# Performance work log

Hardware: AMD Instinct MI355X
Metric: run time of the kernel (lower is better)

## Reference

```python
import jax, jax.numpy as jnp
import numpy as np

B, S, H = 1, 2048, 1024
NH, NKV, HD = 16, 4, 64
E, F, TOPK = 8, 2048, 2
EPS = 1e-6
ALPHA = 1.702
LIMIT = 7.0


def setup_inputs() -> dict:
    key = jax.random.key(0)
    ks = jax.random.split(key, 16)
    sc = 0.02
    inv_freq = 1.0 / (10000.0 ** (jnp.arange(0, HD, 2, dtype=jnp.float32) / HD))  # [HD/2]
    pos = jnp.arange(S, dtype=jnp.float32)[:, None] * inv_freq[None, :]  # [S, HD/2]
    causal = jnp.tril(jnp.ones((S, S), dtype=bool))
    mask = jnp.where(causal, 0.0, -1e9).astype(jnp.float32)[None, None]  # [1,1,S,S]
    return {
        "hidden_states": jax.random.normal(ks[0], (B, S, H), jnp.float32),
        "sins": jnp.sin(pos),
        "coss": jnp.cos(pos),
        "mask": mask,
        "ln1_w": jnp.ones((H,), jnp.float32),
        "ln2_w": jnp.ones((H,), jnp.float32),
        "wq": jax.random.normal(ks[1], (H, NH * HD), jnp.float32) * sc,
        "wk": jax.random.normal(ks[2], (H, NKV * HD), jnp.float32) * sc,
        "wv": jax.random.normal(ks[3], (H, NKV * HD), jnp.float32) * sc,
        "wo": jax.random.normal(ks[4], (NH * HD, H), jnp.float32) * sc,
        "w_router": jax.random.normal(ks[5], (H, E), jnp.float32) * sc,
        "b_router": jnp.zeros((E,), jnp.float32),
        "gate_up_proj": jax.random.normal(ks[6], (E, H, 2 * F), jnp.float32) * sc,
        "gate_up_bias": jnp.zeros((E, 2 * F), jnp.float32),
        "down_proj": jax.random.normal(ks[7], (E, F, H), jnp.float32) * sc,
        "down_bias": jnp.zeros((E, H), jnp.float32),
    }


def _rmsnorm(x, w):
    x = x.astype(jnp.float32)
    var = jnp.mean(x * x, axis=-1, keepdims=True)
    return x * jax.lax.rsqrt(var + EPS) * w


def _rope(x, sins, coss):
    # x: [B, S, nH, HD]; sins/coss: [S, HD/2]
    d = x.shape[-1] // 2
    xr, xi = x[..., :d], x[..., d:]
    s = sins[None, : x.shape[1], None, :]
    c = coss[None, : x.shape[1], None, :]
    return jnp.concatenate([xr * c - xi * s, xr * s + xi * c], axis=-1)


def reference(hidden_states, sins, coss, mask, ln1_w, ln2_w, wq, wk, wv, wo,
              w_router, b_router, gate_up_proj, gate_up_bias, down_proj, down_bias):
    # ---- attention block ----
    residual = hidden_states
    x = _rmsnorm(hidden_states, ln1_w)
    q = (x @ wq).reshape(B, S, NH, HD)
    k = (x @ wk).reshape(B, S, NKV, HD)
    v = (x @ wv).reshape(B, S, NKV, HD)
    q = _rope(q, sins, coss)
    k = _rope(k, sins, coss)
    groups = NH // NKV
    k = jnp.repeat(k, groups, axis=2)  # [B,S,NH,HD]
    v = jnp.repeat(v, groups, axis=2)
    scale = 1.0 / jnp.sqrt(jnp.float32(HD))
    scores = jnp.einsum("bqhd,bkhd->bhqk", q, k) * scale + mask
    probs = jax.nn.softmax(scores, axis=-1)
    attn = jnp.einsum("bhqk,bkhd->bqhd", probs, v).reshape(B, S, NH * HD)
    hidden = residual + attn @ wo

    # ---- MoE block ----
    residual = hidden
    x = _rmsnorm(hidden, ln2_w)
    flat = x.reshape(-1, H)  # [N, H], N = B*S
    logits = flat @ w_router + b_router  # [N, E]
    top_val, top_idx = jax.lax.top_k(logits, TOPK)
    top_val = jax.nn.softmax(top_val, axis=-1)
    scores_r = jnp.zeros_like(logits)
    token_idx = jnp.arange(B * S)[:, None]
    scores_r = scores_r.at[token_idx, top_idx].set(top_val)  # [N, E]

    # dense all-expert FFN (faithful to original)
    gate_up = jnp.einsum("nh,ehd->end", flat, gate_up_proj) + gate_up_bias[:, None, :]
    gate = jnp.minimum(gate_up[..., ::2], LIMIT)
    up = jnp.clip(gate_up[..., 1::2], -LIMIT, LIMIT)
    glu = gate * jax.nn.sigmoid(gate * ALPHA)
    gated = (up + 1.0) * glu  # [E, N, F]
    next_states = jnp.einsum("end,edh->enh", gated, down_proj) + down_bias[:, None, :]
    weights = scores_r.T  # [E, N]
    moe_out = jnp.sum(next_states * weights[..., None], axis=0).reshape(B, S, H)

    return residual + moe_out
```

## Files before the change

kernel.cpp:

```cpp
#include <hip/hip_runtime.h>
#include <hip/hip_bf16.h>
#include <math.h>

#define SS 2048
#define HH 1024
#define NHEADS 16
#define NKVH 4
#define HDIM 64
#define NEXP 8
#define FDIM 2048

static constexpr float EPSV   = 1e-6f;
static constexpr float ALPHAV = 1.702f;
static constexpr float LIMITV = 7.0f;

typedef __attribute__((ext_vector_type(8))) short bf16x8;
typedef __attribute__((ext_vector_type(4))) float f32x4;

__device__ __forceinline__ float wave_reduce_sum(float v) {
#pragma unroll
  for (int off = 32; off; off >>= 1) v += __shfl_xor(v, off);
  return v;
}

__device__ __forceinline__ unsigned short bf16_bits(float x) {
  __hip_bfloat16 h = __float2bfloat16(x);
  return *reinterpret_cast<unsigned short*>(&h);
}

__device__ __forceinline__ float bf16u_to_f(unsigned short u) {
  union { unsigned int i; float f; } c;
  c.i = ((unsigned int)u) << 16;
  return c.f;
}

__device__ __forceinline__ void gload_lds16(const __hip_bfloat16* g, __hip_bfloat16* s) {
  __builtin_amdgcn_global_load_lds(
      (const __attribute__((address_space(1))) void*)g,
      (__attribute__((address_space(3))) void*)s, 16, 0, 0);
}

__global__ void rmsnorm_kernel(const float* __restrict__ x,
                               const float* __restrict__ w,
                               float* __restrict__ o32,
                               __hip_bfloat16* __restrict__ o16) {
  int row = blockIdx.x;
  int t = threadIdx.x;
  const float4 v = ((const float4*)(x + (size_t)row * HH))[t];
  float ss = v.x * v.x + v.y * v.y + v.z * v.z + v.w * v.w;
  ss = wave_reduce_sum(ss);
  __shared__ float parts[4];
  if ((t & 63) == 0) parts[t >> 6] = ss;
  __syncthreads();
  float tot = parts[0] + parts[1] + parts[2] + parts[3];
  float r = rsqrtf(tot * (1.0f / HH) + EPSV);
  const float4 ww = ((const float4*)w)[t];
  float4 out;
  out.x = v.x * r * ww.x;
  out.y = v.y * r * ww.y;
  out.z = v.z * r * ww.z;
  out.w = v.w * r * ww.w;
  if (o32) ((float4*)(o32 + (size_t)row * HH))[t] = out;
  __hip_bfloat16* d = o16 + (size_t)row * HH + t * 4;
  d[0] = __float2bfloat16(out.x);
  d[1] = __float2bfloat16(out.y);
  d[2] = __float2bfloat16(out.z);
  d[3] = __float2bfloat16(out.w);
}

__device__ __forceinline__ void tcast_body(
    const float* __restrict__ ip, __hip_bfloat16* __restrict__ op,
    int R, int C, int bx, int by, int tid) {
  __shared__ float tile[64][65];
  int c0 = bx * 64, r0 = by * 64;
  int tx = tid & 15, ty = tid >> 4;
#pragma unroll
  for (int j = 0; j < 4; ++j) {
    int row = ty + j * 16;
    float4 v = *(const float4*)(ip + (size_t)(r0 + row) * C + c0 + tx * 4);
    tile[row][tx * 4 + 0] = v.x;
    tile[row][tx * 4 + 1] = v.y;
    tile[row][tx * 4 + 2] = v.z;
    tile[row][tx * 4 + 3] = v.w;
  }
  __syncthreads();
#pragma unroll
  for (int j = 0; j < 4; ++j) {
    int crow = ty + j * 16;
    ushort4 o;
    o.x = bf16_bits(tile[tx * 4 + 0][crow]);
    o.y = bf16_bits(tile[tx * 4 + 1][crow]);
    o.z = bf16_bits(tile[tx * 4 + 2][crow]);
    o.w = bf16_bits(tile[tx * 4 + 3][crow]);
    *(ushort4*)(op + (size_t)(c0 + crow) * R + r0 + tx * 4) = o;
  }
}

__global__ __launch_bounds__(256) void tcast_kernel(
    const float* __restrict__ in, __hip_bfloat16* __restrict__ out,
    int R, int C, size_t inBatch, size_t outBatch) {
  tcast_body(in + blockIdx.z * inBatch, out + blockIdx.z * outBatch,
             R, C, blockIdx.x, blockIdx.y, threadIdx.x);
}

__global__ __launch_bounds__(256) void tcast4_kernel(
    const float* __restrict__ wq, const float* __restrict__ wk,
    const float* __restrict__ wv, const float* __restrict__ wo,
    __hip_bfloat16* __restrict__ qkvT, __hip_bfloat16* __restrict__ woT) {
  int z = blockIdx.z;
  const float* in;
  __hip_bfloat16* out;
  int C;
  if (z == 0)      { in = wq; out = qkvT;                C = 1024; }
  else if (z == 1) { in = wk; out = qkvT + 1024 * 1024;  C = 256; }
  else if (z == 2) { in = wv; out = qkvT + 1280 * 1024;  C = 256; }
  else             { in = wo; out = woT;                 C = 1024; }
  if (blockIdx.x * 64 >= C) return;
  tcast_body(in, out, 1024, C, blockIdx.x, blockIdx.y, threadIdx.x);
}

template <int MODE>
__global__ __launch_bounds__(256, 4) void mfma_gemm(
    const __hip_bfloat16* __restrict__ A,
    const __hip_bfloat16* __restrict__ Bt,
    float* __restrict__ Cf, __hip_bfloat16* __restrict__ Cb,
    const float* __restrict__ addend, const float* __restrict__ bias,
    const int* __restrict__ counts, const int* __restrict__ offsets,
    const int* __restrict__ tos, int M0, int N, int K) {
  int e = blockIdx.z;
  int M = M0, off = 0;
  if (MODE >= 2) { M = counts[e]; off = offsets[e]; }
  int row0 = blockIdx.y * 128;
  if (row0 >= M) return;
  int n0 = blockIdx.x * 128;
  const __hip_bfloat16* Bte = Bt + (size_t)e * ((size_t)N * K);
  __shared__ __align__(16) __hip_bfloat16 sA0[128 * 32];
  __shared__ __align__(16) __hip_bfloat16 sA1[128 * 32];
  __shared__ __align__(16) __hip_bfloat16 sB0[128 * 32];
  __shared__ __align__(16) __hip_bfloat16 sB1[128 * 32];
  int t = threadIdx.x;
  int lane = t & 63;
  int wm = t >> 7, wn = (t >> 6) & 1;
  f32x4 acc[4][4] = {};

  int arow[2];
#pragma unroll
  for (int i = 0; i < 2; ++i) {
    int rg = row0 + i * 64 + (t >> 2);
    int ar;
    if (MODE == 2)      ar = (rg < M) ? tos[off + rg] : tos[off];
    else if (MODE == 3) ar = off + ((rg < M) ? rg : 0);
    else                ar = rg;
    arow[i] = ar;
  }
  int brow0 = n0 + (t >> 2);
  int kc = (t & 3) * 8;

  for (int k0 = 0; k0 < K; k0 += 64) {
#pragma unroll
    for (int i = 0; i < 2; ++i) {
      int r = i * 64 + (t >> 2);
      const __hip_bfloat16* ap = A + (size_t)arow[i] * K + k0 + kc;
      const __hip_bfloat16* bp = Bte + (size_t)(brow0 + i * 64) * K + k0 + kc;
      gload_lds16(ap, sA0 + r * 32 + kc);
      gload_lds16(ap + 32, sA1 + r * 32 + kc);
      gload_lds16(bp, sB0 + r * 32 + kc);
      gload_lds16(bp + 32, sB1 + r * 32 + kc);
    }
    __syncthreads();
#pragma unroll
    for (int half = 0; half < 2; ++half) {
      const __hip_bfloat16* sa = half ? sA1 : sA0;
      const __hip_bfloat16* sb = half ? sB1 : sB0;
      bf16x8 af[4], bfr[4];
#pragma unroll
      for (int mi = 0; mi < 4; ++mi)
        af[mi] = *(const bf16x8*)(sa + (wm * 64 + mi * 16 + (lane & 15)) * 32 + (lane >> 4) * 8);
#pragma unroll
      for (int ni = 0; ni < 4; ++ni)
        bfr[ni] = *(const bf16x8*)(sb + (wn * 64 + ni * 16 + (lane & 15)) * 32 + (lane >> 4) * 8);
#pragma unroll
      for (int mi = 0; mi < 4; ++mi)
#pragma unroll
        for (int ni = 0; ni < 4; ++ni)
          acc[mi][ni] = __builtin_amdgcn_mfma_f32_16x16x32_bf16(af[mi], bfr[ni], acc[mi][ni], 0, 0, 0);
    }
    __syncthreads();
  }

#pragma unroll
  for (int mi = 0; mi < 4; ++mi) {
#pragma unroll
    for (int ni = 0; ni < 4; ++ni) {
      int col = n0 + wn * 64 + ni * 16 + (lane & 15);
#pragma unroll
      for (int j = 0; j < 4; ++j) {
        float v = acc[mi][ni][j];
        int rg = row0 + wm * 64 + mi * 16 + (lane >> 4) * 4 + j;
        if (MODE == 0) {
          Cf[(size_t)rg * N + col] = v;
        } else if (MODE == 1) {
          Cf[(size_t)rg * N + col] = v + addend[(size_t)rg * N + col];
        } else if (MODE == 2) {
          float other = __shfl_xor(v, 1);
          if (!(lane & 1) && rg < M) {
            float gate = fminf(v + bias[(size_t)e * N + col], LIMITV);
            float up = fminf(fmaxf(other + bias[(size_t)e * N + col + 1], -LIMITV), LIMITV);
            float glu = gate / (1.f + __expf(-gate * ALPHAV));
            Cb[(size_t)(off + rg) * (N / 2) + (col >> 1)] = __float2bfloat16((up + 1.f) * glu);
          }
        } else {
          if (rg < M)
            Cf[(size_t)(off + rg) * N + col] = v + bias[(size_t)e * N + col];
        }
      }
    }
  }
}

__global__ __launch_bounds__(512) void rope_cast_kernel(
    const float* __restrict__ qkv, const float* __restrict__ sins,
    const float* __restrict__ coss,
    __hip_bfloat16* __restrict__ qhi, __hip_bfloat16* __restrict__ qlo,
    __hip_bfloat16* __restrict__ khi, __hip_bfloat16* __restrict__ klo) {
  int s = blockIdx.x, t = threadIdx.x;
  const float* rowp = qkv + (size_t)s * 1536;
  int hh = t >> 5, j = t & 31;
  float c = coss[s * 32 + j], sn = sins[s * 32 + j];
  {
    float xr = rowp[hh * 64 + j], xi = rowp[hh * 64 + 32 + j];
    float y0 = xr * c - xi * sn;
    float y1 = xr * sn + xi * c;
    size_t i0 = (size_t)s * 1024 + hh * 64 + j;
    __hip_bfloat16 h0 = __float2bfloat16(y0);
    __hip_bfloat16 h1 = __float2bfloat16(y1);
    qhi[i0] = h0;      qlo[i0] = __float2bfloat16(y0 - __bfloat162float(h0));
    qhi[i0 + 32] = h1; qlo[i0 + 32] = __float2bfloat16(y1 - __bfloat162float(h1));
  }
  if (t < 128) {
    int kh = t >> 5;
    float xr = rowp[1024 + kh * 64 + j], xi = rowp[1024 + kh * 64 + 32 + j];
    float y0 = xr * c - xi * sn;
    float y1 = xr * sn + xi * c;
    size_t i0 = (size_t)kh * 131072 + s * 64 + j;
    __hip_bfloat16 h0 = __float2bfloat16(y0);
    __hip_bfloat16 h1 = __float2bfloat16(y1);
    khi[i0] = h0;      klo[i0] = __float2bfloat16(y0 - __bfloat162float(h0));
    khi[i0 + 32] = h1; klo[i0 + 32] = __float2bfloat16(y1 - __bfloat162float(h1));
  }
}

__global__ void vtrans_kernel(const float* __restrict__ qkv,
                              __hip_bfloat16* __restrict__ vT,
                              int* __restrict__ counts) {
  if (blockIdx.x == 0 && blockIdx.y == 0 && blockIdx.z == 0 && threadIdx.x < 8)
    counts[threadIdx.x] = 0;
  __shared__ float tile[32][33];
  int kh = blockIdx.z;
  int d0 = blockIdx.x * 32;
  int s0 = blockIdx.y * 32;
  int tx = threadIdx.x & 31, ty = threadIdx.x >> 5;
#pragma unroll
  for (int j = 0; j < 4; ++j)
    tile[ty * 4 + j][tx] =
        qkv[(size_t)(s0 + ty * 4 + j) * 1536 + 1280 + kh * 64 + d0 + tx];
  __syncthreads();
#pragma unroll
  for (int j = 0; j < 4; ++j)
    vT[(size_t)kh * 131072 + (size_t)(d0 + ty * 4 + j) * 2048 + s0 + tx] =
        __float2bfloat16(tile[tx][ty * 4 + j]);
}

__device__ __forceinline__ void swsm(
    f32x4* sacc, float (*p)[4], int kv0, bool last, int qr, int g,
    float& m, float& l, float* af4, f32x4* acc_o) {
  float smax = -1e30f;
#pragma unroll
  for (int n = 0; n < 4; ++n)
#pragma unroll
    for (int j = 0; j < 4; ++j) {
      float s = sacc[n][j] * 0.125f;
      if (last && (kv0 + n * 16 + g * 4 + j) > qr) s = -1e30f;
      p[n][j] = s;
      smax = fmaxf(smax, s);
    }
  smax = fmaxf(smax, __shfl_xor(smax, 16));
  smax = fmaxf(smax, __shfl_xor(smax, 32));
  float mnew = fmaxf(m, smax);
  float a = __expf(m - mnew);
  float rs = 0.f;
#pragma unroll
  for (int n = 0; n < 4; ++n)
#pragma unroll
    for (int j = 0; j < 4; ++j) {
      float e2 = __expf(p[n][j] - mnew);
      p[n][j] = e2;
      rs += e2;
    }
  rs += __shfl_xor(rs, 16);
  rs += __shfl_xor(rs, 32);
  l = l * a + rs;
  m = mnew;
#pragma unroll
  for (int j = 0; j < 4; ++j) af4[j] = __shfl(a, g * 4 + j);
#pragma unroll
  for (int n2 = 0; n2 < 4; ++n2)
#pragma unroll
    for (int j = 0; j < 4; ++j) acc_o[n2][j] *= af4[j];
}

__device__ __forceinline__ void build_pfrag(
    float (*p)[4], int s2, int H0, int H1, int nsel, bf16x8& Ah, bf16x8& Al) {
  unsigned int pkh[2][2], pkl[2][2];
#pragma unroll
  for (int nn = 0; nn < 2; ++nn) {
#pragma unroll
    for (int d = 0; d < 2; ++d) {
      float p0 = p[2 * s2 + nn][2 * d], p1 = p[2 * s2 + nn][2 * d + 1];
      unsigned short h0 = bf16_bits(p0), h1 = bf16_bits(p1);
      pkh[nn][d] = (unsigned int)h0 | ((unsigned int)h1 << 16);
      float l0 = p0 - bf16u_to_f(h0), l1 = p1 - bf16u_to_f(h1);
      pkl[nn][d] = (unsigned int)bf16_bits(l0) | ((unsigned int)bf16_bits(l1) << 16);
    }
  }
  union { unsigned int u[4]; bf16x8 v; } AhU, AlU;
#pragma unroll
  for (int d = 0; d < 2; ++d) {
    unsigned int x0 = (unsigned int)__shfl((int)pkh[0][d], H0);
    unsigned int x1 = (unsigned int)__shfl((int)pkh[1][d], H0);
    AhU.u[d] = nsel ? x1 : x0;
    unsigned int y0 = (unsigned int)__shfl((int)pkh[0][d], H1);
    unsigned int y1 = (unsigned int)__shfl((int)pkh[1][d], H1);
    AhU.u[2 + d] = nsel ? y1 : y0;
    unsigned int z0 = (unsigned int)__shfl((int)pkl[0][d], H0);
    unsigned int z1 = (unsigned int)__shfl((int)pkl[1][d], H0);
    AlU.u[d] = nsel ? z1 : z0;
    unsigned int w0 = (unsigned int)__shfl((int)pkl[0][d], H1);
    unsigned int w1 = (unsigned int)__shfl((int)pkl[1][d], H1);
    AlU.u[2 + d] = nsel ? w1 : w0;
  }
  Ah = AhU.v;
  Al = AlU.v;
}

__global__ __launch_bounds__(128) void mfma_attn(
    const __hip_bfloat16* __restrict__ qhi, const __hip_bfloat16* __restrict__ qlo,
    const __hip_bfloat16* __restrict__ khi, const __hip_bfloat16* __restrict__ klo,
    const __hip_bfloat16* __restrict__ vT,
    float* __restrict__ pacc,
    float* __restrict__ pm,
    float* __restrict__ pl) {
  int hp = blockIdx.y;
  int h0 = 2 * hp, h1 = 2 * hp + 1, kh = hp >> 1;
  int ck = blockIdx.z;
  int wq = threadIdx.x >> 6;
  int qb = 2 * blockIdx.x + wq;
  if (16 * ck > qb) return;
  int lane = threadIdx.x & 63;
  int g = lane >> 4, q = lane & 15;
  int qrow0 = qb * 16;
  const int koff = g * 8;

  bf16x8 bqhA[2], bqlA[2], bqhB[2], bqlB[2];
  {
    size_t qoA = (size_t)(qrow0 + q) * 1024 + h0 * 64;
    bqhA[0] = *(const bf16x8*)(qhi + qoA + koff);
    bqhA[1] = *(const bf16x8*)(qhi + qoA + 32 + koff);
    bqlA[0] = *(const bf16x8*)(qlo + qoA + koff);
    bqlA[1] = *(const bf16x8*)(qlo + qoA + 32 + koff);
    size_t qoB = qoA + 64;
    bqhB[0] = *(const bf16x8*)(qhi + qoB + koff);
    bqhB[1] = *(const bf16x8*)(qhi + qoB + 32 + koff);
    bqlB[0] = *(const bf16x8*)(qlo + qoB + koff);
    bqlB[1] = *(const bf16x8*)(qlo + qoB + 32 + koff);
  }
  f32x4 accA[4] = {}, accB[4] = {};
  float mA = -1e30f, lA = 0.f, mB = -1e30f, lB = 0.f;
  const size_t kbase = (size_t)kh * (SS * 64) + (size_t)q * 64 + koff;
  const __hip_bfloat16* khp = khi + kbase;
  const __hip_bfloat16* klp = klo + kbase;
  const __hip_bfloat16* vfp =
      vT + (size_t)kh * (64 * SS) + (size_t)q * SS + koff;

  int ntiles = qb / 4 + 1;
  int lastT = ntiles - 1;
  int t0 = 4 * ck;
  int t1 = 4 * ck + 4; if (t1 > ntiles) t1 = ntiles;

  const int H0s = ((2 * g) & 3) * 16 + q;
  const int H1s = ((2 * g + 1) & 3) * 16 + q;
  const int nsel = (g >> 1) & 1;
  int qr = qrow0 + q;

  for (int tile = t0; tile < t1; ++tile) {
    int kv0 = tile * 64;
    bool last = (tile == lastT);

    bf16x8 kfh[4][2], kfl[4][2];
#pragma unroll
    for (int n = 0; n < 4; ++n)
#pragma unroll
      for (int step = 0; step < 2; ++step) {
        size_t ko = (size_t)(kv0 + n * 16) * 64 + step * 32;
        kfh[n][step] = *(const bf16x8*)(khp + ko);
        kfl[n][step] = *(const bf16x8*)(klp + ko);
      }

    f32x4 sA[4] = {}, sB[4] = {};
    __builtin_amdgcn_s_setprio(1);
#pragma unroll
    for (int n = 0; n < 4; ++n) {
#pragma unroll
      for (int step = 0; step < 2; ++step) {
        sA[n] = __builtin_amdgcn_mfma_f32_16x16x32_bf16(kfh[n][step], bqhA[step], sA[n], 0, 0, 0);
        sB[n] = __builtin_amdgcn_mfma_f32_16x16x32_bf16(kfh[n][step], bqhB[step], sB[n], 0, 0, 0);
        sA[n] = __builtin_amdgcn_mfma_f32_16x16x32_bf16(kfl[n][step], bqhA[step], sA[n], 0, 0, 0);
        sB[n] = __builtin_amdgcn_mfma_f32_16x16x32_bf16(kfl[n][step], bqhB[step], sB[n], 0, 0, 0);
        sA[n] = __builtin_amdgcn_mfma_f32_16x16x32_bf16(kfh[n][step], bqlA[step], sA[n], 0, 0, 0);
        sB[n] = __builtin_amdgcn_mfma_f32_16x16x32_bf16(kfh[n][step], bqlB[step], sB[n], 0, 0, 0);
      }
    }
    __builtin_amdgcn_s_setprio(0);

    bf16x8 vf[4][2];
#pragma unroll
    for (int s2 = 0; s2 < 2; ++s2)
#pragma unroll
      for (int n2 = 0; n2 < 4; ++n2)
        vf[n2][s2] = *(const bf16x8*)(vfp + (size_t)(n2 * 16) * SS + kv0 + s2 * 32);

    float pA[4][4], pB[4][4];
    float af4[4];
    swsm(sA, pA, kv0, last, qr, g, mA, lA, af4, accA);
    swsm(sB, pB, kv0, last, qr, g, mB, lB, af4, accB);

#pragma unroll
    for (int s2 = 0; s2 < 2; ++s2) {
      bf16x8 AhA, AlA, AhB, AlB;
      build_pfrag(pA, s2, H0s, H1s, nsel, AhA, AlA);
      build_pfrag(pB, s2, H0s, H1s, nsel, AhB, AlB);
      __builtin_amdgcn_s_setprio(1);
#pragma unroll
      for (int n2 = 0; n2 < 4; ++n2) {
        accA[n2] = __builtin_amdgcn_mfma_f32_16x16x32_bf16(AhA, vf[n2][s2], accA[n2], 0, 0, 0);
        accB[n2] = __builtin_amdgcn_mfma_f32_16x16x32_bf16(AhB, vf[n2][s2], accB[n2], 0, 0, 0);
        accA[n2] = __builtin_amdgcn_mfma_f32_16x16x32_bf16(AlA, vf[n2][s2], accA[n2], 0, 0, 0);
        accB[n2] = __builtin_amdgcn_mfma_f32_16x16x32_bf16(AlB, vf[n2][s2], accB[n2], 0, 0, 0);
      }
      __builtin_amdgcn_s_setprio(0);
    }
  }

#pragma unroll
  for (int n2 = 0; n2 < 4; ++n2) {
#pragma unroll
    for (int j = 0; j < 4; ++j) {
      int row = qrow0 + g * 4 + j;
      size_t base = ((size_t)ck * SS + row) * 1024 + n2 * 16 + q;
      pacc[base + h0 * 64] = accA[n2][j];
      pacc[base + h1 * 64] = accB[n2][j];
    }
  }
  if (lane < 16) {
    pm[(ck * 16 + h0) * SS + qrow0 + lane] = mA;
    pl[(ck * 16 + h0) * SS + qrow0 + lane] = lA;
  } else if (lane < 32) {
    pm[(ck * 16 + h1) * SS + qrow0 + (lane - 16)] = mB;
    pl[(ck * 16 + h1) * SS + qrow0 + (lane - 16)] = lB;
  }
}

__global__ __launch_bounds__(256) void attn_merge(
    const float* __restrict__ pacc, const float* __restrict__ pm,
    const float* __restrict__ pl, __hip_bfloat16* __restrict__ o) {
  int r = blockIdx.x;
  int t = threadIdx.x;
  int col = t * 4;
  int h = col >> 6;
  int nch = r / 256 + 1;
  float M = -1e30f;
  for (int c = 0; c < nch; ++c) M = fmaxf(M, pm[(c * 16 + h) * SS + r]);
  float L = 0.f;
  float4 acc = {0.f, 0.f, 0.f, 0.f};
  for (int c = 0; c < nch; ++c) {
    float w = __expf(pm[(c * 16 + h) * SS + r] - M);
    L += w * pl[(c * 16 + h) * SS + r];
    float4 a = *(const float4*)(pacc + ((size_t)c * SS + r) * 1024 + col);
    acc.x += w * a.x; acc.y += w * a.y; acc.z += w * a.z; acc.w += w * a.w;
  }
  float inv = 1.f / L;
  __hip_bfloat16* d = o + (size_t)r * 1024 + col;
  d[0] = __float2bfloat16(acc.x * inv);
  d[1] = __float2bfloat16(acc.y * inv);
  d[2] = __float2bfloat16(acc.z * inv);
  d[3] = __float2bfloat16(acc.w * inv);
}

__global__ __launch_bounds__(256) void router_kernel(
    const float* __restrict__ xn2, const float* __restrict__ wr,
    const float* __restrict__ br,
    int* __restrict__ tok_e, float* __restrict__ tok_w,
    int* __restrict__ counts) {
  int wv = threadIdx.x >> 6, lane = threadIdx.x & 63;
  int tok = blockIdx.x * 4 + wv;
  const float* x = xn2 + (size_t)tok * HH;
  float acc[NEXP] = {};
#pragma unroll
  for (int p = 0; p < 4; ++p) {
    int d0 = p * 256 + lane * 4;
    float4 xv = *(const float4*)(x + d0);
    float xs[4] = {xv.x, xv.y, xv.z, xv.w};
#pragma unroll
    for (int dd = 0; dd < 4; ++dd) {
      const float4* wrow = (const float4*)(wr + (size_t)(d0 + dd) * NEXP);
      float4 w0 = wrow[0], w1 = wrow[1];
      acc[0] += xs[dd] * w0.x; acc[1] += xs[dd] * w0.y;
      acc[2] += xs[dd] * w0.z; acc[3] += xs[dd] * w0.w;
      acc[4] += xs[dd] * w1.x; acc[5] += xs[dd] * w1.y;
      acc[6] += xs[dd] * w1.z; acc[7] += xs[dd] * w1.w;
    }
  }
  float lg[NEXP];
#pragma unroll
  for (int e = 0; e < NEXP; ++e) lg[e] = wave_reduce_sum(acc[e]) + br[e];
  if (lane == 0) {
    int e0 = 0; float v0 = lg[0];
#pragma unroll
    for (int e = 1; e < NEXP; ++e) if (lg[e] > v0) { v0 = lg[e]; e0 = e; }
    int e1 = -1; float v1 = -1e30f;
#pragma unroll
    for (int e = 0; e < NEXP; ++e)
      if (e != e0 && lg[e] > v1) { v1 = lg[e]; e1 = e; }
    float z = __expf(v1 - v0);
    float w0 = 1.f / (1.f + z);
    tok_e[2 * tok] = e0; tok_e[2 * tok + 1] = e1;
    tok_w[2 * tok] = w0; tok_w[2 * tok + 1] = 1.f - w0;
    atomicAdd(&counts[e0], 1);
    atomicAdd(&counts[e1], 1);
  }
}

__global__ void offsets_kernel(const int* __restrict__ counts,
                               int* __restrict__ offsets, int* __restrict__ cursor) {
  int s = 0;
#pragma unroll
  for (int e = 0; e < NEXP; ++e) { offsets[e] = s; s += counts[e]; cursor[e] = 0; }
}

__global__ void scatter_kernel(const int* __restrict__ tok_e,
                               const int* __restrict__ offsets, int* __restrict__ cursor,
                               int* __restrict__ token_of_slot,
                               int* __restrict__ slot_of_token) {
  int tok = blockIdx.x * 64 + threadIdx.x;
#pragma unroll
  for (int s2 = 0; s2 < 2; ++s2) {
    int e = tok_e[2 * tok + s2];
    int pos = atomicAdd(&cursor[e], 1);
    int g = offsets[e] + pos;
    token_of_slot[g] = tok;
    slot_of_token[2 * tok + s2] = g;
  }
}

__global__ void combine_kernel(const float* __restrict__ resid2,
                               const float* __restrict__ dout,
                               const int* __restrict__ slot_of_token,
                               const float* __restrict__ tok_w,
                               float* __restrict__ out) {
  int tok = blockIdx.x;
  int g0 = slot_of_token[2 * tok], g1 = slot_of_token[2 * tok + 1];
  float w0 = tok_w[2 * tok], w1 = tok_w[2 * tok + 1];
  int i = threadIdx.x;
  float4 r = ((const float4*)(resid2 + (size_t)tok * HH))[i];
  float4 a = ((const float4*)(dout + (size_t)g0 * HH))[i];
  float4 b = ((const float4*)(dout + (size_t)g1 * HH))[i];
  float4 o;
  o.x = r.x + w0 * a.x + w1 * b.x;
  o.y = r.y + w0 * a.y + w1 * b.y;
  o.z = r.z + w0 * a.z + w1 * b.z;
  o.w = r.w + w0 * a.w + w1 * b.w;
  ((float4*)(out + (size_t)tok * HH))[i] = o;
}

extern "C" void kernel_launch(void* const* d_in, const int* in_sizes, int n_in,
                              void* d_out, int out_size, void* d_ws, size_t ws_size,
                              hipStream_t stream) {
  const float* hidden = (const float*)d_in[0];
  const float* sins   = (const float*)d_in[1];
  const float* coss   = (const float*)d_in[2];
  const float* ln1_w  = (const float*)d_in[4];
  const float* ln2_w  = (const float*)d_in[5];
  const float* wq     = (const float*)d_in[6];
  const float* wk     = (const float*)d_in[7];
  const float* wv     = (const float*)d_in[8];
  const float* wo     = (const float*)d_in[9];
  const float* w_router = (const float*)d_in[10];
  const float* b_router = (const float*)d_in[11];
  const float* gup    = (const float*)d_in[12];
  const float* gub    = (const float*)d_in[13];
  const float* dp     = (const float*)d_in[14];
  const float* db     = (const float*)d_in[15];
  float* out = (float*)d_out;

  float* ws = (float*)d_ws;
  float* resid2 = ws;
  float* xn2    = resid2 + 2097152;
  __hip_bfloat16* xn2b = (__hip_bfloat16*)(xn2 + 2097152);
  float* pa = xn2 + 2097152 + 1048576;
  __hip_bfloat16* xn1b = (__hip_bfloat16*)pa;
  __hip_bfloat16* qlo_b = (__hip_bfloat16*)pa;
  float* qkv = pa + 1048576;
  __hip_bfloat16* qkvT = (__hip_bfloat16*)(pa + 4194304);
  __hip_bfloat16* woT  = qkvT + 1572864;
  __hip_bfloat16* qhi_b = (__hip_bfloat16*)(pa + 5505024);
  __hip_bfloat16* khi_b = qhi_b + 2097152;
  __hip_bfloat16* vTb  = khi_b + 524288;
  __hip_bfloat16* attnb = (__hip_bfloat16*)(pa + 7077888);
  __hip_bfloat16* klo_b = (__hip_bfloat16*)(pa + 8126464);
  __hip_bfloat16* dpT = (__hip_bfloat16*)pa;
  float* pb = pa + 8388608;
  __hip_bfloat16* gupT = (__hip_bfloat16*)pb;
  float* pacc = pb;
  float* pm_b = pb + 16777216;
  float* pl_b = pm_b + 262144;
  __hip_bfloat16* gatedb = gupT + 33554432;
  float* dout = pb + 16777216 + 4194304;
  float* tok_w = dout + 4194304;
  int* counts = (int*)(tok_w + 4096);
  int* offsets = counts + 8;
  int* cursor = offsets + 8;
  int* tok_e = cursor + 8;
  int* token_of_slot = tok_e + 4096;
  int* slot_of_token = token_of_slot + 4096;

  rmsnorm_kernel<<<SS, 256, 0, stream>>>(hidden, ln1_w, nullptr, xn1b);
  tcast4_kernel<<<dim3(16, 16, 4), 256, 0, stream>>>(wq, wk, wv, wo, qkvT, woT);
  mfma_gemm<0><<<dim3(12, 16, 1), 256, 0, stream>>>(
      xn1b, qkvT, qkv, nullptr, nullptr, nullptr, nullptr, nullptr, nullptr, SS, 1536, 1024);
  rope_cast_kernel<<<SS, 512, 0, stream>>>(qkv, sins, coss, qhi_b, qlo_b, khi_b, klo_b);
  vtrans_kernel<<<dim3(2, 64, 4), 256, 0, stream>>>(qkv, vTb, counts);
  mfma_attn<<<dim3(64, 8, 8), 128, 0, stream>>>(
      qhi_b, qlo_b, khi_b, klo_b, vTb, pacc, pm_b, pl_b);
  attn_merge<<<SS, 256, 0, stream>>>(pacc, pm_b, pl_b, attnb);
  mfma_gemm<1><<<dim3(8, 16, 1), 256, 0, stream>>>(
      attnb, woT, resid2, nullptr, hidden, nullptr, nullptr, nullptr, nullptr, SS, 1024, 1024);
  rmsnorm_kernel<<<SS, 256, 0, stream>>>(resid2, ln2_w, xn2, xn2b);
  tcast_kernel<<<dim3(16, 32, NEXP), 256, 0, stream>>>(
      dp, dpT, 2048, 1024, (size_t)2048 * 1024, (size_t)1024 * 2048);
  tcast_kernel<<<dim3(64, 16, NEXP), 256, 0, stream>>>(
      gup, gupT, 1024, 4096, (size_t)1024 * 4096, (size_t)4096 * 1024);
  router_kernel<<<SS / 4, 256, 0, stream>>>(xn2, w_router, b_router, tok_e, tok_w, counts);
  offsets_kernel<<<1, 1, 0, stream>>>(counts, offsets, cursor);
  scatter_kernel<<<SS / 64, 64, 0, stream>>>(tok_e, offsets, cursor, token_of_slot, slot_of_token);
  mfma_gemm<2><<<dim3(32, 16, NEXP), 256, 0, stream>>>(
      xn2b, gupT, nullptr, gatedb, nullptr, gub, counts, offsets, token_of_slot, 0, 4096, 1024);
  mfma_gemm<3><<<dim3(8, 16, NEXP), 256, 0, stream>>>(
      gatedb, dpT, dout, nullptr, nullptr, db, counts, offsets, nullptr, 0, 1024, 2048);
  combine_kernel<<<SS, 256, 0, stream>>>(resid2, dout, slot_of_token, tok_w, out);
}
```

Before: 439.2 us.

## Double-buffer GEMM K-loop with async LDS prefetch and merge MoE weight casts

The GEMM main loop now splits each 64-wide K step into 32-wide stages held in two LDS buffers. It prefetches the next stage with direct global-to-LDS loads and uses a partial vmcnt wait plus raw s_barrier, so memory traffic overlaps the MFMA work instead of fully synchronising every iteration. Separately, the two MoE weight transpose-cast launches are fused into one kernel with a larger grid to save a launch. The cost is twice as many barriers per K, and many blocks in the fused grid exit immediately.

```diff
diff --git a/kernel.cpp b/kernel.cpp
--- a/kernel.cpp
+++ b/kernel.cpp
@@ -96,13 +96,6 @@
   }
 }
 
-__global__ __launch_bounds__(256) void tcast_kernel(
-    const float* __restrict__ in, __hip_bfloat16* __restrict__ out,
-    int R, int C, size_t inBatch, size_t outBatch) {
-  tcast_body(in + blockIdx.z * inBatch, out + blockIdx.z * outBatch,
-             R, C, blockIdx.x, blockIdx.y, threadIdx.x);
-}
-
 __global__ __launch_bounds__(256) void tcast4_kernel(
     const float* __restrict__ wq, const float* __restrict__ wk,
     const float* __restrict__ wv, const float* __restrict__ wo,
@@ -117,6 +110,22 @@
   else             { in = wo; out = woT;                 C = 1024; }
   if (blockIdx.x * 64 >= C) return;
   tcast_body(in, out, 1024, C, blockIdx.x, blockIdx.y, threadIdx.x);
+}
+
+__global__ __launch_bounds__(256) void tcast_moe_kernel(
+    const float* __restrict__ dp, const float* __restrict__ gup,
+    __hip_bfloat16* __restrict__ dpT, __hip_bfloat16* __restrict__ gupT) {
+  int z = blockIdx.z;
+  if (z < 8) {
+    if (blockIdx.x >= 16) return;
+    tcast_body(dp + (size_t)z * 2048 * 1024, dpT + (size_t)z * 1024 * 2048,
+               2048, 1024, blockIdx.x, blockIdx.y, threadIdx.x);
+  } else {
+    if (blockIdx.y >= 16) return;
+    tcast_body(gup + (size_t)(z - 8) * 1024 * 4096,
+               gupT + (size_t)(z - 8) * 4096 * 1024,
+               1024, 4096, blockIdx.x, blockIdx.y, threadIdx.x);
+  }
 }
 
 template <int MODE>
@@ -134,10 +143,8 @@
   if (row0 >= M) return;
   int n0 = blockIdx.x * 128;
   const __hip_bfloat16* Bte = Bt + (size_t)e * ((size_t)N * K);
-  __shared__ __align__(16) __hip_bfloat16 sA0[128 * 32];
-  __shared__ __align__(16) __hip_bfloat16 sA1[128 * 32];
-  __shared__ __align__(16) __hip_bfloat16 sB0[128 * 32];
-  __shared__ __align__(16) __hip_bfloat16 sB1[128 * 32];
+  __shared__ __align__(16) __hip_bfloat16 sA[2][128 * 32];
+  __shared__ __align__(16) __hip_bfloat16 sB[2][128 * 32];
   int t = threadIdx.x;
   int lane = t & 63;
   int wm = t >> 7, wn = (t >> 6) & 1;
@@ -155,23 +162,35 @@
   }
   int brow0 = n0 + (t >> 2);
   int kc = (t & 3) * 8;
-
-  for (int k0 = 0; k0 < K; k0 += 64) {
-#pragma unroll
-    for (int i = 0; i < 2; ++i) {
-      int r = i * 64 + (t >> 2);
-      const __hip_bfloat16* ap = A + (size_t)arow[i] * K + k0 + kc;
-      const __hip_bfloat16* bp = Bte + (size_t)(brow0 + i * 64) * K + k0 + kc;
-      gload_lds16(ap, sA0 + r * 32 + kc);
-      gload_lds16(ap + 32, sA1 + r * 32 + kc);
-      gload_lds16(bp, sB0 + r * 32 + kc);
-      gload_lds16(bp + 32, sB1 + r * 32 + kc);
-    }
-    __syncthreads();
-#pragma unroll
-    for (int half = 0; half < 2; ++half) {
-      const __hip_bfloat16* sa = half ? sA1 : sA0;
-      const __hip_bfloat16* sb = half ? sB1 : sB0;
+  int rt = t >> 2;
+  const __hip_bfloat16* aBase0 = A + (size_t)arow[0] * K + kc;
+  const __hip_bfloat16* aBase1 = A + (size_t)arow[1] * K + kc;
+  const __hip_bfloat16* bBase0 = Bte + (size_t)brow0 * K + kc;
+  const __hip_bfloat16* bBase1 = Bte + (size_t)(brow0 + 64) * K + kc;
+
+#define STAGE_HALF(buf, s)                                                 \
+  do {                                                                     \
+    int kk_ = (s) * 32;                                                    \
+    gload_lds16(aBase0 + kk_, sA[buf] + rt * 32 + kc);                     \
+    gload_lds16(bBase0 + kk_, sB[buf] + rt * 32 + kc);                     \
+    gload_lds16(aBase1 + kk_, sA[buf] + (64 + rt) * 32 + kc);              \
+    gload_lds16(bBase1 + kk_, sB[buf] + (64 + rt) * 32 + kc);              \
+  } while (0)
+
+  int nsteps = K / 32;
+  STAGE_HALF(0, 0);
+  for (int s = 0; s < nsteps; ++s) {
+    int cur = s & 1;
+    if (s + 1 < nsteps) {
+      STAGE_HALF(cur ^ 1, s + 1);
+      asm volatile("s_waitcnt vmcnt(4)" ::: "memory");
+    } else {
+      asm volatile("s_waitcnt vmcnt(0)" ::: "memory");
+    }
+    asm volatile("s_barrier" ::: "memory");
+    {
+      const __hip_bfloat16* sa = sA[cur];
+      const __hip_bfloat16* sb = sB[cur];
       bf16x8 af[4], bfr[4];
 #pragma unroll
       for (int mi = 0; mi < 4; ++mi)
@@ -185,8 +204,9 @@
         for (int ni = 0; ni < 4; ++ni)
           acc[mi][ni] = __builtin_amdgcn_mfma_f32_16x16x32_bf16(af[mi], bfr[ni], acc[mi][ni], 0, 0, 0);
     }
-    __syncthreads();
-  }
+    asm volatile("s_barrier" ::: "memory");
+  }
+#undef STAGE_HALF
 
 #pragma unroll
   for (int mi = 0; mi < 4; ++mi) {
@@ -645,10 +665,7 @@
   mfma_gemm<1><<<dim3(8, 16, 1), 256, 0, stream>>>(
       attnb, woT, resid2, nullptr, hidden, nullptr, nullptr, nullptr, nullptr, SS, 1024, 1024);
   rmsnorm_kernel<<<SS, 256, 0, stream>>>(resid2, ln2_w, xn2, xn2b);
-  tcast_kernel<<<dim3(16, 32, NEXP), 256, 0, stream>>>(
-      dp, dpT, 2048, 1024, (size_t)2048 * 1024, (size_t)1024 * 2048);
-  tcast_kernel<<<dim3(64, 16, NEXP), 256, 0, stream>>>(
-      gup, gupT, 1024, 4096, (size_t)1024 * 4096, (size_t)4096 * 1024);
+  tcast_moe_kernel<<<dim3(64, 32, 16), 256, 0, stream>>>(dp, gup, dpT, gupT);
   router_kernel<<<SS / 4, 256, 0, stream>>>(xn2, w_router, b_router, tok_e, tok_w, counts);
   offsets_kernel<<<1, 1, 0, stream>>>(counts, offsets, cursor);
   scatter_kernel<<<SS / 64, 64, 0, stream>>>(tok_e, offsets, cursor, token_of_slot, slot_of_token);
```

Result: slower. 462.2 us (+5.3%).
